# Kernel tuning notes

Measured on AMD Instinct MI355X. Metric: run time of the kernel, lower is better.

## Reference

```python
import jax, jax.numpy as jnp
import numpy as np

C = 1024   # hidden_size
H = 16     # num_heads
D = C // H # head dim
M = 4096   # mlp hidden
T = 1024   # motion seq len
B = 8      # batch
TA = 1024  # audio seq len


def _w(key, shape):
    return jax.random.normal(key, shape, dtype=jnp.float32) * 0.02


def setup_inputs() -> dict:
    key = jax.random.key(0)
    ks = jax.random.split(key, 32)
    inp = {
        'x': jax.random.normal(ks[0], (T, B, C), dtype=jnp.float32),
        'c': jax.random.normal(ks[1], (B, C), dtype=jnp.float32),
        'padding_mask': jax.random.randint(ks[2], (B, T), 0, 2, dtype=jnp.int32),
        'audio_seq': jax.random.normal(ks[3], (TA, B, C), dtype=jnp.float32),
        'audio_mask': jax.random.randint(ks[4], (B, TA), 0, 2, dtype=jnp.int32),
        # adaLN modulation: SiLU -> Linear(C, 6C)
        'w_ada': _w(ks[5], (C, 6 * C)), 'b_ada': jnp.zeros((6 * C,), jnp.float32),
        # self-attention q/k/v/proj
        'wq': _w(ks[6], (C, C)), 'bq': jnp.zeros((C,), jnp.float32),
        'wk': _w(ks[7], (C, C)), 'bk': jnp.zeros((C,), jnp.float32),
        'wv': _w(ks[8], (C, C)), 'bv': jnp.zeros((C,), jnp.float32),
        'wo': _w(ks[9], (C, C)), 'bo': jnp.zeros((C,), jnp.float32),
        # cross-attention q/k/v/proj
        'cwq': _w(ks[10], (C, C)), 'cbq': jnp.zeros((C,), jnp.float32),
        'cwk': _w(ks[11], (C, C)), 'cbk': jnp.zeros((C,), jnp.float32),
        'cwv': _w(ks[12], (C, C)), 'cbv': jnp.zeros((C,), jnp.float32),
        'cwo': _w(ks[13], (C, C)), 'cbo': jnp.zeros((C,), jnp.float32),
        # MLP fc1/fc2
        'w1': _w(ks[14], (C, M)), 'b1': jnp.zeros((M,), jnp.float32),
        'w2': _w(ks[15], (M, C)), 'b2': jnp.zeros((C,), jnp.float32),
    }
    return inp


def _ln(x):
    # LayerNorm(elementwise_affine=False, eps=1e-6)
    mu = jnp.mean(x, axis=-1, keepdims=True)
    var = jnp.var(x, axis=-1, keepdims=True)
    return (x - mu) * jax.lax.rsqrt(var + 1e-6)


def _modulate(x, shift, scale):
    # batch-first x [B, T, C]; shift/scale [B, C]
    return x * (1.0 + scale[:, None, :]) + shift[:, None, :]


def _mha(xq, xkv, wq, bq, wk, bk, wv, bv, wo, bo, mask):
    # xq [B, Tq, C], xkv [B, Tk, C], mask [B, Tk] (nonzero = masked)
    b, tq, _ = xq.shape
    tk = xkv.shape[1]
    q = (xq @ wq + bq).reshape(b, tq, H, D)
    k = (xkv @ wk + bk).reshape(b, tk, H, D)
    v = (xkv @ wv + bv).reshape(b, tk, H, D)
    att = jnp.einsum('bqhd,bkhd->bhqk', q, k) * (1.0 / np.sqrt(D))
    att = jnp.where(mask[:, None, None, :] != 0, -jnp.inf, att)
    att = jax.nn.softmax(att, axis=-1)
    y = jnp.einsum('bhqk,bkhd->bqhd', att, v).reshape(b, tq, C)
    return y @ wo + bo


def _gelu_tanh(x):
    return jax.nn.gelu(x, approximate=True)


def reference(x, c, padding_mask, audio_seq, audio_mask,
              w_ada, b_ada, wq, bq, wk, bk, wv, bv, wo, bo,
              cwq, cbq, cwk, cbk, cwv, cbv, cwo, cbo,
              w1, b1, w2, b2):
    # adaLN modulation parameters
    mod = jax.nn.silu(c) @ w_ada + b_ada                 # [B, 6C]
    (shift_msa, scale_msa, gate_msa,
     shift_mlp, scale_mlp, gate_mlp) = jnp.split(mod, 6, axis=1)

    # x is sequence-first [T, B, C] (padding_mask batch dim matches x dim 1)
    x_batch = jnp.transpose(x, (1, 0, 2))                # [B, T, C]
    x_mod = _modulate(_ln(x_batch), shift_msa, scale_msa)
    attn_out = _mha(x_mod, x_mod, wq, bq, wk, bk, wv, bv, wo, bo, padding_mask)
    x = x + gate_msa[None, :, :] * jnp.transpose(attn_out, (1, 0, 2))

    # cross attention (reuses msa shift/scale/gate, as in the source)
    xb = jnp.transpose(x, (1, 0, 2))                     # [B, T, C]
    ab = jnp.transpose(audio_seq, (1, 0, 2))             # [B, TA, C]
    x_cross_in = _modulate(_ln(xb), shift_msa, scale_msa)
    cross_out = _mha(x_cross_in, ab, cwq, cbq, cwk, cbk, cwv, cbv, cwo, cbo,
                     audio_mask)
    x = x + gate_msa[None, :, :] * jnp.transpose(cross_out, (1, 0, 2))

    # MLP
    xb = jnp.transpose(x, (1, 0, 2))
    h = _modulate(_ln(xb), shift_mlp, scale_mlp)
    mlp_out = _gelu_tanh(h @ w1 + b1) @ w2 + b2
    x = x + gate_mlp[None, :, :] * jnp.transpose(mlp_out, (1, 0, 2))
    return x
```

## Files before the change

kernel.cpp:

```cpp
#include <hip/hip_runtime.h>
#include <math.h>

#define T_SEQ 1024
#define TA_SEQ 1024
#define BATCH 8
#define CH 1024
#define NH 16
#define HD 64
#define MH 4096

typedef unsigned short u16;
typedef unsigned short u16x4 __attribute__((ext_vector_type(4)));
typedef unsigned short u16x8 __attribute__((ext_vector_type(8)));
typedef __bf16 bf16x8 __attribute__((ext_vector_type(8)));
typedef float f32x4 __attribute__((ext_vector_type(4)));

__device__ __forceinline__ u16 f2bf(float f) {
  unsigned int u = __builtin_bit_cast(unsigned int, f);
  u += 0x7FFFu + ((u >> 16) & 1u);
  return (u16)(u >> 16);
}
__device__ __forceinline__ u16 f2bf_trunc(float f) {
  return (u16)(__builtin_bit_cast(unsigned int, f) >> 16);
}
__device__ __forceinline__ bf16x8 ldbf8(const u16* p) {
  return __builtin_bit_cast(bf16x8, *reinterpret_cast<const u16x8*>(p));
}
__device__ __forceinline__ void gload_lds16(const u16* g, u16* l) {
  __builtin_amdgcn_global_load_lds(
      (const __attribute__((address_space(1))) unsigned int*)g,
      (__attribute__((address_space(3))) unsigned int*)l, 16, 0, 0);
}

__global__ void k_transpose_w(const float* __restrict__ in, u16* __restrict__ out,
                              int K, int N) {
  __shared__ float tile[32][33];
  int n0 = blockIdx.x * 32, k0 = blockIdx.y * 32;
  int tx = threadIdx.x, ty = threadIdx.y;
#pragma unroll
  for (int i = 0; i < 4; i++)
    tile[ty + i * 8][tx] = in[(size_t)(k0 + ty + i * 8) * N + n0 + tx];
  __syncthreads();
#pragma unroll
  for (int i = 0; i < 4; i++)
    out[(size_t)(n0 + ty + i * 8) * K + k0 + tx] = f2bf(tile[tx][ty + i * 8]);
}

struct P8f { const float* p[8]; };
struct P8u { u16* p[8]; };
__global__ void k_transpose8(P8f in8, P8u out8) {
  const float* __restrict__ in = in8.p[blockIdx.z];
  u16* __restrict__ out = out8.p[blockIdx.z];
  __shared__ float tile[32][33];
  int n0 = blockIdx.x * 32, k0 = blockIdx.y * 32;
  int tx = threadIdx.x, ty = threadIdx.y;
#pragma unroll
  for (int i = 0; i < 4; i++)
    tile[ty + i * 8][tx] = in[(size_t)(k0 + ty + i * 8) * CH + n0 + tx];
  __syncthreads();
#pragma unroll
  for (int i = 0; i < 4; i++)
    out[(size_t)(n0 + ty + i * 8) * CH + k0 + tx] = f2bf(tile[tx][ty + i * 8]);
}

__global__ void k_ada(const float* __restrict__ c, const float* __restrict__ w_ada,
                      const float* __restrict__ b_ada, float* __restrict__ mod) {
  __shared__ float sc[CH];
  int b = blockIdx.y;
  int tid = threadIdx.x;
  for (int i = tid; i < CH; i += 256) {
    float cv = c[b * CH + i];
    sc[i] = cv / (1.0f + expf(-cv));
  }
  __syncthreads();
  int n = blockIdx.x * 256 + tid;
  float acc = 0.0f;
  for (int k = 0; k < CH; k++) acc += sc[k] * w_ada[(size_t)k * (6 * CH) + n];
  mod[(size_t)b * (6 * CH) + n] = acc + b_ada[n];
}

__global__ void k_tbc_to_btc_f32(const float* __restrict__ in, float* __restrict__ out) {
  size_t i = (size_t)blockIdx.x * 256 + threadIdx.x;
  int c = (int)(i & (CH - 1));
  size_t tb = i >> 10;
  int b = (int)(tb & (BATCH - 1));
  size_t t = tb >> 3;
  out[((size_t)b * T_SEQ + t) * CH + c] = in[i];
}
__global__ void k_tbc_to_btc_bf16(const float* __restrict__ in, u16* __restrict__ out) {
  size_t i = (size_t)blockIdx.x * 256 + threadIdx.x;
  int c = (int)(i & (CH - 1));
  size_t tb = i >> 10;
  int b = (int)(tb & (BATCH - 1));
  size_t t = tb >> 3;
  out[((size_t)b * TA_SEQ + t) * CH + c] = f2bf(in[i]);
}

__global__ void k_ln_mod(const float* __restrict__ xb, const float* __restrict__ mod,
                         u16* __restrict__ out, int shift_sel, int scale_sel) {
  int row = blockIdx.x;
  int b = row >> 10;
  int tid = threadIdx.x;
  const float* xr = xb + (size_t)row * CH;
  float4 v = reinterpret_cast<const float4*>(xr)[tid];
  float s = v.x + v.y + v.z + v.w;
  float s2 = v.x * v.x + v.y * v.y + v.z * v.z + v.w * v.w;
#pragma unroll
  for (int off = 32; off > 0; off >>= 1) {
    s += __shfl_down(s, off);
    s2 += __shfl_down(s2, off);
  }
  __shared__ float red[8];
  __shared__ float stats[2];
  int wid = tid >> 6;
  if ((tid & 63) == 0) { red[wid] = s; red[4 + wid] = s2; }
  __syncthreads();
  if (tid == 0) {
    float a = red[0] + red[1] + red[2] + red[3];
    float a2 = red[4] + red[5] + red[6] + red[7];
    float mu = a * (1.0f / CH);
    float var = a2 * (1.0f / CH) - mu * mu;
    stats[0] = mu;
    stats[1] = rsqrtf(var + 1e-6f);
  }
  __syncthreads();
  float mu = stats[0], rs = stats[1];
  int c0 = tid * 4;
  const float* sh = mod + (size_t)b * (6 * CH) + (size_t)shift_sel * CH + c0;
  const float* scl = mod + (size_t)b * (6 * CH) + (size_t)scale_sel * CH + c0;
  float xs[4] = {v.x, v.y, v.z, v.w};
  u16x4 o;
#pragma unroll
  for (int j = 0; j < 4; j++)
    o[j] = f2bf((xs[j] - mu) * rs * (1.0f + scl[j]) + sh[j]);
  *reinterpret_cast<u16x4*>(out + (size_t)row * CH + c0) = o;
}

__device__ __forceinline__ void gemm_compute(const u16* As, const u16* Bs,
                                             int wm, int wn, int lrow, int sx,
                                             f32x4 (&acc)[4][4]) {
  bf16x8 af[4], bfr[4];
#pragma unroll
  for (int mi = 0; mi < 4; mi++)
    af[mi] = ldbf8(&As[(wm + mi * 16 + lrow) * 32 + sx]);
#pragma unroll
  for (int ni = 0; ni < 4; ni++)
    bfr[ni] = ldbf8(&Bs[(wn + ni * 16 + lrow) * 32 + sx]);
#pragma unroll
  for (int mi = 0; mi < 4; mi++)
#pragma unroll
    for (int ni = 0; ni < 4; ni++)
      acc[mi][ni] = __builtin_amdgcn_mfma_f32_16x16x32_bf16(af[mi], bfr[ni],
                                                            acc[mi][ni], 0, 0, 0);
}

__device__ __forceinline__ void gemm_core(
    const u16* __restrict__ A, const u16* __restrict__ Bt, int K,
    int m0, int n0, int tid, u16* As, u16* Bs, f32x4 (&acc)[4][4]) {
  int wid = tid >> 6, lane = tid & 63;
  int wm = (wid >> 1) * 64, wn = (wid & 1) * 64;
  int lrow = lane & 15, quad = lane >> 4;
  int sx = (quad ^ ((lrow >> 1) & 3)) * 8;
  int c0 = tid, c1 = 256 + tid;
  int r0 = c0 >> 2, r1 = c1 >> 2;
  int q0 = ((c0 & 3) ^ ((r0 >> 1) & 3)) * 8;
  int q1 = ((c1 & 3) ^ ((r1 >> 1) & 3)) * 8;
  const u16* ga0 = A + (size_t)(m0 + r0) * K + q0;
  const u16* ga1 = A + (size_t)(m0 + r1) * K + q1;
  const u16* gb0 = Bt + (size_t)(n0 + r0) * K + q0;
  const u16* gb1 = Bt + (size_t)(n0 + r1) * K + q1;
  u16* la0 = As + c0 * 8;
  u16* la1 = As + c1 * 8;
  u16* lb0 = Bs + c0 * 8;
  u16* lb1 = Bs + c1 * 8;
  const int kiters = K >> 5;
  gload_lds16(ga0, la0);
  gload_lds16(ga1, la1);
  gload_lds16(gb0, lb0);
  gload_lds16(gb1, lb1);
  __syncthreads();
  for (int kt = 0; kt < kiters; kt += 2) {
    {
      int ke = (kt + 1) << 5;
      gload_lds16(ga0 + ke, la0 + 4096);
      gload_lds16(ga1 + ke, la1 + 4096);
      gload_lds16(gb0 + ke, lb0 + 4096);
      gload_lds16(gb1 + ke, lb1 + 4096);
    }
    gemm_compute(As, Bs, wm, wn, lrow, sx, acc);
    __syncthreads();
    if (kt + 2 < kiters) {
      int ko = (kt + 2) << 5;
      gload_lds16(ga0 + ko, la0);
      gload_lds16(ga1 + ko, la1);
      gload_lds16(gb0 + ko, lb0);
      gload_lds16(gb1 + ko, lb1);
    }
    gemm_compute(As + 4096, Bs + 4096, wm, wn, lrow, sx, acc);
    if (kt + 2 < kiters) __syncthreads();
  }
}

template <int EPI>
__global__ __launch_bounds__(256) void k_gemm(
    const u16* __restrict__ A, const u16* __restrict__ Bt,
    const float* __restrict__ bias, u16* __restrict__ out_bf,
    float* __restrict__ xb, const float* __restrict__ mod, int gate_sel,
    int M, int N, int K) {
  __shared__ u16 As[2 * 128 * 32];
  __shared__ u16 Bs[2 * 128 * 32];
  int m0 = blockIdx.x * 128, n0 = blockIdx.y * 128;
  int tid = threadIdx.x;
  int wid = tid >> 6, lane = tid & 63;
  int wm = (wid >> 1) * 64, wn = (wid & 1) * 64;
  int lrow = lane & 15, quad = lane >> 4;
  f32x4 acc[4][4];
#pragma unroll
  for (int mi = 0; mi < 4; mi++)
#pragma unroll
    for (int ni = 0; ni < 4; ni++) acc[mi][ni] = {0.f, 0.f, 0.f, 0.f};
  gemm_core(A, Bt, K, m0, n0, tid, As, Bs, acc);
#pragma unroll
  for (int mi = 0; mi < 4; mi++)
#pragma unroll
    for (int ni = 0; ni < 4; ni++) {
      int col = n0 + wn + ni * 16 + lrow;
      float bval = bias[col];
#pragma unroll
      for (int r = 0; r < 4; r++) {
        int row = m0 + wm + mi * 16 + quad * 4 + r;
        float v = acc[mi][ni][r] + bval;
        if (EPI == 1) {
          int b = row >> 10;
          float g = mod[(size_t)b * (6 * CH) + (size_t)gate_sel * CH + col];
          xb[(size_t)row * N + col] += g * v;
        } else if (EPI == 2) {
          float t = 0.79788456080286536f * (v + 0.044715f * v * v * v);
          float gel = 0.5f * v * (1.0f + tanhf(t));
          out_bf[(size_t)row * N + col] = f2bf(gel);
        } else {
          out_bf[(size_t)row * N + col] = f2bf(v * 0.18033688011112042f);
        }
      }
    }
}

__global__ __launch_bounds__(256) void k_gemm_qkv(
    const u16* __restrict__ A, const u16* __restrict__ Bt,
    const float* __restrict__ bq, const float* __restrict__ bk,
    const float* __restrict__ bv,
    u16* __restrict__ qout, u16* __restrict__ kout, u16* __restrict__ vt) {
  __shared__ u16 As[2 * 128 * 32];
  __shared__ u16 Bs[2 * 128 * 32];
  int m0 = blockIdx.x * 128, n0 = blockIdx.y * 128;
  int tid = threadIdx.x;
  int wid = tid >> 6, lane = tid & 63;
  int wm = (wid >> 1) * 64, wn = (wid & 1) * 64;
  int lrow = lane & 15, quad = lane >> 4;
  f32x4 acc[4][4];
#pragma unroll
  for (int mi = 0; mi < 4; mi++)
#pragma unroll
    for (int ni = 0; ni < 4; ni++) acc[mi][ni] = {0.f, 0.f, 0.f, 0.f};
  gemm_core(A, Bt, CH, m0, n0, tid, As, Bs, acc);
  int seg = n0 >> 10;
  const float* bias = (seg == 0) ? bq : (seg == 1) ? bk : bv;
#pragma unroll
  for (int mi = 0; mi < 4; mi++)
#pragma unroll
    for (int ni = 0; ni < 4; ni++) {
      int col = (n0 & 1023) + wn + ni * 16 + lrow;
      float bval = bias[col];
      int row0 = m0 + wm + mi * 16 + quad * 4;
      if (seg == 0) {
#pragma unroll
        for (int r = 0; r < 4; r++)
          qout[(size_t)(row0 + r) * CH + col] =
              f2bf((acc[mi][ni][r] + bval) * 0.18033688011112042f);
      } else if (seg == 1) {
#pragma unroll
        for (int r = 0; r < 4; r++)
          kout[(size_t)(row0 + r) * CH + col] = f2bf(acc[mi][ni][r] + bval);
      } else {
        u16x4 pk;
#pragma unroll
        for (int r = 0; r < 4; r++) pk[r] = f2bf(acc[mi][ni][r] + bval);
        int b = row0 >> 10, t0 = row0 & 1023;
        int h = col >> 6, d = col & 63;
        *reinterpret_cast<u16x4*>(
            vt + (((size_t)(b * NH + h) * HD + d) << 10) + t0) = pk;
      }
    }
}

__global__ __launch_bounds__(256) void k_gemm_kv(
    const u16* __restrict__ A, const u16* __restrict__ Bt,
    const float* __restrict__ bk, const float* __restrict__ bv,
    u16* __restrict__ kout, u16* __restrict__ vt) {
  __shared__ u16 As[2 * 128 * 32];
  __shared__ u16 Bs[2 * 128 * 32];
  int m0 = blockIdx.x * 128, n0 = blockIdx.y * 128;
  int tid = threadIdx.x;
  int wid = tid >> 6, lane = tid & 63;
  int wm = (wid >> 1) * 64, wn = (wid & 1) * 64;
  int lrow = lane & 15, quad = lane >> 4;
  f32x4 acc[4][4];
#pragma unroll
  for (int mi = 0; mi < 4; mi++)
#pragma unroll
    for (int ni = 0; ni < 4; ni++) acc[mi][ni] = {0.f, 0.f, 0.f, 0.f};
  gemm_core(A, Bt, CH, m0, n0, tid, As, Bs, acc);
  int seg = n0 >> 10;
  const float* bias = (seg == 0) ? bk : bv;
#pragma unroll
  for (int mi = 0; mi < 4; mi++)
#pragma unroll
    for (int ni = 0; ni < 4; ni++) {
      int col = (n0 & 1023) + wn + ni * 16 + lrow;
      float bval = bias[col];
      int row0 = m0 + wm + mi * 16 + quad * 4;
      if (seg == 0) {
#pragma unroll
        for (int r = 0; r < 4; r++)
          kout[(size_t)(row0 + r) * CH + col] = f2bf(acc[mi][ni][r] + bval);
      } else {
        u16x4 pk;
#pragma unroll
        for (int r = 0; r < 4; r++) pk[r] = f2bf(acc[mi][ni][r] + bval);
        int b = row0 >> 10, t0 = row0 & 1023;
        int h = col >> 6, d = col & 63;
        *reinterpret_cast<u16x4*>(
            vt + (((size_t)(b * NH + h) * HD + d) << 10) + t0) = pk;
      }
    }
}

__global__ __launch_bounds__(256, 2) void k_attn(
    const u16* __restrict__ Q, const u16* __restrict__ Kb,
    const u16* __restrict__ vt, const int* __restrict__ mask,
    u16* __restrict__ Y) {
  int qt = blockIdx.x, h = blockIdx.y, b = blockIdx.z;
  int tid = threadIdx.x, wid = tid >> 6, lane = tid & 63;
  int lrow = lane & 15, quad = lane >> 4;
  int qbase = qt * 256 + wid * 64;

  __shared__ u16 P[4][4][16][72];

  bf16x8 aq[4][2];
#pragma unroll
  for (int st = 0; st < 4; st++) {
    size_t qoff = ((size_t)(b * T_SEQ + qbase + st * 16 + lrow)) * CH + h * HD;
    aq[st][0] = ldbf8(Q + qoff + quad * 8);
    aq[st][1] = ldbf8(Q + qoff + 32 + quad * 8);
  }

  u16x8 uo;
#pragma unroll
  for (int j = 0; j < 8; j++) uo[j] = (lrow == 0) ? (u16)0x3F80 : (u16)0;
  bf16x8 ones = __builtin_bit_cast(bf16x8, uo);

  const int* mrow = mask + (size_t)b * T_SEQ;
  const u16* ksrc = Kb + ((size_t)(b * T_SEQ) + lrow) * CH + h * HD + quad * 8;
  const u16* vsrc = vt + (((size_t)(b * NH + h) * HD + lrow) << 10) + quad * 8;

  f32x4 o[4][5];
#pragma unroll
  for (int st = 0; st < 4; st++)
#pragma unroll
    for (int dc = 0; dc < 5; dc++) o[st][dc] = {0.f, 0.f, 0.f, 0.f};

  for (int kt = 0; kt < 16; kt++) {
    int kb = kt * 64;
    bf16x8 kf[8];
    float mb[4];
#pragma unroll
    for (int sub = 0; sub < 4; sub++) {
      const u16* kp = ksrc + (size_t)(kb + sub * 16) * CH;
      kf[sub * 2] = ldbf8(kp);
      kf[sub * 2 + 1] = ldbf8(kp + 32);
      mb[sub] = mrow[kb + sub * 16 + lrow] ? -INFINITY : 0.0f;
    }
    bf16x8 vf[8];
#pragma unroll
    for (int dc = 0; dc < 4; dc++) {
      const u16* vp = vsrc + (size_t)(dc * 16) * 1024 + kb;
      vf[dc * 2] = ldbf8(vp);
      vf[dc * 2 + 1] = ldbf8(vp + 32);
    }
#pragma unroll
    for (int st = 0; st < 4; st++) {
#pragma unroll
      for (int sub = 0; sub < 4; sub++) {
        f32x4 z = {0.f, 0.f, 0.f, 0.f};
        z = __builtin_amdgcn_mfma_f32_16x16x32_bf16(aq[st][0], kf[sub * 2], z, 0, 0, 0);
        z = __builtin_amdgcn_mfma_f32_16x16x32_bf16(aq[st][1], kf[sub * 2 + 1], z, 0, 0, 0);
        float mbv = mb[sub];
#pragma unroll
        for (int r = 0; r < 4; r++) {
          float p = exp2f(z[r] + mbv);
          P[wid][st][quad * 4 + r][sub * 16 + lrow] = f2bf_trunc(p);
        }
      }
    }
#pragma unroll
    for (int st = 0; st < 4; st++) {
      bf16x8 pf0 = ldbf8(&P[wid][st][lrow][quad * 8]);
      bf16x8 pf1 = ldbf8(&P[wid][st][lrow][32 + quad * 8]);
#pragma unroll
      for (int dc = 0; dc < 4; dc++) {
        o[st][dc] = __builtin_amdgcn_mfma_f32_16x16x32_bf16(pf0, vf[dc * 2], o[st][dc], 0, 0, 0);
        o[st][dc] = __builtin_amdgcn_mfma_f32_16x16x32_bf16(pf1, vf[dc * 2 + 1], o[st][dc], 0, 0, 0);
      }
      o[st][4] = __builtin_amdgcn_mfma_f32_16x16x32_bf16(pf0, ones, o[st][4], 0, 0, 0);
      o[st][4] = __builtin_amdgcn_mfma_f32_16x16x32_bf16(pf1, ones, o[st][4], 0, 0, 0);
    }
  }

#pragma unroll
  for (int st = 0; st < 4; st++)
#pragma unroll
    for (int r = 0; r < 4; r++) {
      float l = __shfl(o[st][4][r], lane & 48);
      float linv = 1.0f / l;
      int qr = qbase + st * 16 + quad * 4 + r;
      size_t yo = ((size_t)(b * T_SEQ + qr)) * CH + h * HD;
#pragma unroll
      for (int dc = 0; dc < 4; dc++)
        Y[yo + dc * 16 + lrow] = f2bf(o[st][dc][r] * linv);
    }
}

__global__ void k_out(const float* __restrict__ xb, float* __restrict__ out) {
  size_t i = (size_t)blockIdx.x * 256 + threadIdx.x;
  int c = (int)(i & (CH - 1));
  size_t tb = i >> 10;
  int b = (int)(tb & (BATCH - 1));
  size_t t = tb >> 3;
  out[i] = xb[((size_t)b * T_SEQ + t) * CH + c];
}

extern "C" void kernel_launch(void* const* d_in, const int* in_sizes, int n_in,
                              void* d_out, int out_size, void* d_ws, size_t ws_size,
                              hipStream_t stream) {
  const float* x     = (const float*)d_in[0];
  const float* c     = (const float*)d_in[1];
  const int*   pmask = (const int*)d_in[2];
  const float* audio = (const float*)d_in[3];
  const int*   amask = (const int*)d_in[4];
  const float* w_ada = (const float*)d_in[5];
  const float* b_ada = (const float*)d_in[6];
  const float* wq = (const float*)d_in[7];  const float* bq = (const float*)d_in[8];
  const float* wk = (const float*)d_in[9];  const float* bk = (const float*)d_in[10];
  const float* wv = (const float*)d_in[11]; const float* bv = (const float*)d_in[12];
  const float* wo = (const float*)d_in[13]; const float* bo = (const float*)d_in[14];
  const float* cwq = (const float*)d_in[15]; const float* cbq = (const float*)d_in[16];
  const float* cwk = (const float*)d_in[17]; const float* cbk = (const float*)d_in[18];
  const float* cwv = (const float*)d_in[19]; const float* cbv = (const float*)d_in[20];
  const float* cwo = (const float*)d_in[21]; const float* cbo = (const float*)d_in[22];
  const float* w1 = (const float*)d_in[23]; const float* b1 = (const float*)d_in[24];
  const float* w2 = (const float*)d_in[25]; const float* b2 = (const float*)d_in[26];

  char* wsb = (char*)d_ws;
  size_t off = 0;
  auto alloc = [&](size_t bytes) {
    char* p = wsb + off;
    off += (bytes + 255) & ~(size_t)255;
    return p;
  };
  const size_t SQ = (size_t)CH * CH * 2;
  u16* wqT  = (u16*)alloc(SQ);
  u16* wkT  = (u16*)alloc(SQ);
  u16* wvT  = (u16*)alloc(SQ);
  u16* woT  = (u16*)alloc(SQ);
  u16* cwqT = (u16*)alloc(SQ);
  u16* cwkT = (u16*)alloc(SQ);
  u16* cwvT = (u16*)alloc(SQ);
  u16* cwoT = (u16*)alloc(SQ);
  u16* w1T  = (u16*)alloc((size_t)CH * MH * 2);
  u16* w2T  = (u16*)alloc((size_t)CH * MH * 2);
  float* mod = (float*)alloc((size_t)BATCH * 6 * CH * 4);
  float* xb  = (float*)alloc((size_t)BATCH * T_SEQ * CH * 4);
  u16* xm    = (u16*)alloc((size_t)BATCH * T_SEQ * CH * 2);
  u16* hbuf  = (u16*)alloc((size_t)BATCH * T_SEQ * MH * 2);
  u16* qbuf  = hbuf;
  u16* kbuf  = hbuf + (size_t)BATCH * T_SEQ * CH;
  u16* ybuf  = hbuf + (size_t)2 * BATCH * T_SEQ * CH;
  u16* vt    = hbuf + (size_t)3 * BATCH * T_SEQ * CH;
  u16* abuf  = (u16*)alloc((size_t)BATCH * TA_SEQ * CH * 2);
  (void)ws_size; (void)in_sizes; (void)n_in; (void)out_size;

  const int NE = T_SEQ * BATCH * CH;
  dim3 tb32(32, 8);

  P8f src8; P8u dst8;
  src8.p[0] = wq;  dst8.p[0] = wqT;
  src8.p[1] = wk;  dst8.p[1] = wkT;
  src8.p[2] = wv;  dst8.p[2] = wvT;
  src8.p[3] = wo;  dst8.p[3] = woT;
  src8.p[4] = cwq; dst8.p[4] = cwqT;
  src8.p[5] = cwk; dst8.p[5] = cwkT;
  src8.p[6] = cwv; dst8.p[6] = cwvT;
  src8.p[7] = cwo; dst8.p[7] = cwoT;
  k_transpose8<<<dim3(CH / 32, CH / 32, 8), tb32, 0, stream>>>(src8, dst8);
  k_transpose_w<<<dim3(MH / 32, CH / 32), tb32, 0, stream>>>(w1, w1T, CH, MH);
  k_transpose_w<<<dim3(CH / 32, MH / 32), tb32, 0, stream>>>(w2, w2T, MH, CH);

  k_ada<<<dim3(6 * CH / 256, BATCH), 256, 0, stream>>>(c, w_ada, b_ada, mod);
  k_tbc_to_btc_f32<<<NE / 256, 256, 0, stream>>>(x, xb);
  k_tbc_to_btc_bf16<<<NE / 256, 256, 0, stream>>>(audio, abuf);

  k_ln_mod<<<BATCH * T_SEQ, 256, 0, stream>>>(xb, mod, xm, 0, 1);
  k_gemm_qkv<<<dim3(64, 24), 256, 0, stream>>>(xm, wqT, bq, bk, bv, qbuf, kbuf, vt);
  k_attn<<<dim3(T_SEQ / 256, NH, BATCH), 256, 0, stream>>>(qbuf, kbuf, vt, pmask, ybuf);
  k_gemm<1><<<dim3(64, 8), 256, 0, stream>>>(ybuf, woT, bo, nullptr, xb, mod, 2, 8192, CH, CH);

  k_ln_mod<<<BATCH * T_SEQ, 256, 0, stream>>>(xb, mod, xm, 0, 1);
  k_gemm<3><<<dim3(64, 8), 256, 0, stream>>>(xm, cwqT, cbq, qbuf, nullptr, nullptr, 0, 8192, CH, CH);
  k_gemm_kv<<<dim3(64, 16), 256, 0, stream>>>(abuf, cwkT, cbk, cbv, kbuf, vt);
  k_attn<<<dim3(T_SEQ / 256, NH, BATCH), 256, 0, stream>>>(qbuf, kbuf, vt, amask, ybuf);
  k_gemm<1><<<dim3(64, 8), 256, 0, stream>>>(ybuf, cwoT, cbo, nullptr, xb, mod, 2, 8192, CH, CH);

  k_ln_mod<<<BATCH * T_SEQ, 256, 0, stream>>>(xb, mod, xm, 3, 4);
  k_gemm<2><<<dim3(64, 32), 256, 0, stream>>>(xm, w1T, b1, hbuf, nullptr, nullptr, 0, 8192, MH, CH);
  k_gemm<1><<<dim3(64, 8), 256, 0, stream>>>(hbuf, w2T, b2, nullptr, xb, mod, 5, 8192, CH, MH);

  k_out<<<NE / 256, 256, 0, stream>>>(xb, (float*)d_out);
}
```

Baseline: 1.010 ms.

## Triple-buffer GEMM LDS pipeline with explicit waitcnt barriers and cheaper GELU

Replaces the double-buffered global-to-LDS GEMM main loop with a three-stage ring buffer. It uses explicit s_waitcnt vmcnt/lgkmcnt plus s_barrier, so two tiles stay in flight while one is computed, instead of full __syncthreads that drain all loads. This raises LDS use per block from 32KB to 48KB, which may cut occupancy. It also rewrites the tanh-GELU epilogue as x*sigmoid(2t) using exp2 and a hardware reciprocal, which changes rounding slightly. The loop assumes kiters is at least 5, with (kiters-2) divisible by 3 for the tail; K=1024 gives 32 iterations and K=4096 gives 128, both of which fit.

```diff
diff --git a/kernel.cpp b/kernel.cpp
--- a/kernel.cpp
+++ b/kernel.cpp
@@ -31,6 +31,11 @@
       (const __attribute__((address_space(1))) unsigned int*)g,
       (__attribute__((address_space(3))) unsigned int*)l, 16, 0, 0);
 }
+
+#define ASM_BAR()   asm volatile("s_barrier" ::: "memory")
+#define ASM_VM4()   asm volatile("s_waitcnt vmcnt(4)" ::: "memory")
+#define ASM_VM0()   asm volatile("s_waitcnt vmcnt(0)" ::: "memory")
+#define ASM_LGKM0() asm volatile("s_waitcnt lgkmcnt(0)" ::: "memory")
 
 __global__ void k_transpose_w(const float* __restrict__ in, u16* __restrict__ out,
                               int K, int N) {
@@ -173,32 +178,32 @@
   u16* la1 = As + c1 * 8;
   u16* lb0 = Bs + c0 * 8;
   u16* lb1 = Bs + c1 * 8;
+  auto stage = [&](int tile, int boff) {
+    int ko = tile << 5;
+    gload_lds16(ga0 + ko, la0 + boff);
+    gload_lds16(ga1 + ko, la1 + boff);
+    gload_lds16(gb0 + ko, lb0 + boff);
+    gload_lds16(gb1 + ko, lb1 + boff);
+  };
   const int kiters = K >> 5;
-  gload_lds16(ga0, la0);
-  gload_lds16(ga1, la1);
-  gload_lds16(gb0, lb0);
-  gload_lds16(gb1, lb1);
-  __syncthreads();
-  for (int kt = 0; kt < kiters; kt += 2) {
-    {
-      int ke = (kt + 1) << 5;
-      gload_lds16(ga0 + ke, la0 + 4096);
-      gload_lds16(ga1 + ke, la1 + 4096);
-      gload_lds16(gb0 + ke, lb0 + 4096);
-      gload_lds16(gb1 + ke, lb1 + 4096);
-    }
+  stage(0, 0);
+  stage(1, 4096);
+  int kt = 0;
+  for (; kt + 4 < kiters; kt += 3) {
+    ASM_LGKM0(); ASM_VM4(); ASM_BAR();
+    stage(kt + 2, 8192);
     gemm_compute(As, Bs, wm, wn, lrow, sx, acc);
-    __syncthreads();
-    if (kt + 2 < kiters) {
-      int ko = (kt + 2) << 5;
-      gload_lds16(ga0 + ko, la0);
-      gload_lds16(ga1 + ko, la1);
-      gload_lds16(gb0 + ko, lb0);
-      gload_lds16(gb1 + ko, lb1);
-    }
+    ASM_LGKM0(); ASM_VM4(); ASM_BAR();
+    stage(kt + 3, 0);
     gemm_compute(As + 4096, Bs + 4096, wm, wn, lrow, sx, acc);
-    if (kt + 2 < kiters) __syncthreads();
+    ASM_LGKM0(); ASM_VM4(); ASM_BAR();
+    stage(kt + 4, 4096);
+    gemm_compute(As + 8192, Bs + 8192, wm, wn, lrow, sx, acc);
   }
+  ASM_LGKM0(); ASM_VM4(); ASM_BAR();
+  gemm_compute(As, Bs, wm, wn, lrow, sx, acc);
+  ASM_LGKM0(); ASM_VM0(); ASM_BAR();
+  gemm_compute(As + 4096, Bs + 4096, wm, wn, lrow, sx, acc);
 }
 
 template <int EPI>
@@ -207,8 +212,8 @@
     const float* __restrict__ bias, u16* __restrict__ out_bf,
     float* __restrict__ xb, const float* __restrict__ mod, int gate_sel,
     int M, int N, int K) {
-  __shared__ u16 As[2 * 128 * 32];
-  __shared__ u16 Bs[2 * 128 * 32];
+  __shared__ u16 As[3 * 128 * 32];
+  __shared__ u16 Bs[3 * 128 * 32];
   int m0 = blockIdx.x * 128, n0 = blockIdx.y * 128;
   int tid = threadIdx.x;
   int wid = tid >> 6, lane = tid & 63;
@@ -235,8 +240,8 @@
           float g = mod[(size_t)b * (6 * CH) + (size_t)gate_sel * CH + col];
           xb[(size_t)row * N + col] += g * v;
         } else if (EPI == 2) {
-          float t = 0.79788456080286536f * (v + 0.044715f * v * v * v);
-          float gel = 0.5f * v * (1.0f + tanhf(t));
+          float t2 = 2.3021181302f * (v + 0.044715f * v * v * v);
+          float gel = v * __builtin_amdgcn_rcpf(1.0f + exp2f(-t2));
           out_bf[(size_t)row * N + col] = f2bf(gel);
         } else {
           out_bf[(size_t)row * N + col] = f2bf(v * 0.18033688011112042f);
@@ -250,8 +255,8 @@
     const float* __restrict__ bq, const float* __restrict__ bk,
     const float* __restrict__ bv,
     u16* __restrict__ qout, u16* __restrict__ kout, u16* __restrict__ vt) {
-  __shared__ u16 As[2 * 128 * 32];
-  __shared__ u16 Bs[2 * 128 * 32];
+  __shared__ u16 As[3 * 128 * 32];
+  __shared__ u16 Bs[3 * 128 * 32];
   int m0 = blockIdx.x * 128, n0 = blockIdx.y * 128;
   int tid = threadIdx.x;
   int wid = tid >> 6, lane = tid & 63;
@@ -297,8 +302,8 @@
     const u16* __restrict__ A, const u16* __restrict__ Bt,
     const float* __restrict__ bk, const float* __restrict__ bv,
     u16* __restrict__ kout, u16* __restrict__ vt) {
-  __shared__ u16 As[2 * 128 * 32];
-  __shared__ u16 Bs[2 * 128 * 32];
+  __shared__ u16 As[3 * 128 * 32];
+  __shared__ u16 Bs[3 * 128 * 32];
   int m0 = blockIdx.x * 128, n0 = blockIdx.y * 128;
   int tid = threadIdx.x;
   int wid = tid >> 6, lane = tid & 63;
```

After: 927.3 us. 1.09x faster.
